# Optimization experiments

Measured on AMD Instinct MI355X. Metric: run time of the kernel, lower is better.

## Reference

```python
import jax, jax.numpy as jnp
import numpy as np

P = 2; NH = 16; HS = 1024; NL = 12; NC = 1000
B, D, H, W = 32, 64, 32, 32
LFEAT = P * P * D  # 256 per-patch feature dim


def _sincos_1d(dim, pos):
    omega = np.arange(dim // 2, dtype=np.float64) / (dim / 2.0)
    omega = 1.0 / 10000 ** omega
    out = np.einsum('m,d->md', pos.reshape(-1), omega)
    return np.concatenate([np.sin(out), np.cos(out)], axis=1)


def _pos_embed(dim, grid_size):
    g = np.arange(grid_size, dtype=np.float32)
    grid = np.stack(np.meshgrid(g, g), axis=0).reshape(2, 1, grid_size, grid_size)
    emb = np.concatenate([_sincos_1d(dim // 2, grid[0]), _sincos_1d(dim // 2, grid[1])], axis=1)
    return jnp.asarray(emb, dtype=jnp.float32)


def setup_inputs() -> dict:
    key = jax.random.key(0)
    ks = iter(jax.random.split(key, 40))
    def w(shape, s=0.02):
        return jax.random.normal(next(ks), shape, jnp.float32) * s
    return {
        'x': jax.random.normal(next(ks), (B, D, H, W), jnp.float32),
        'y': jax.random.randint(next(ks), (B,), 0, NC),
        't': jax.random.randint(next(ks), (B,), 0, 1000),
        'proj_w': w((LFEAT, HS)), 'proj_b': jnp.zeros((HS,), jnp.float32),
        'pos_embed': _pos_embed(HS, H // P),
        'emb_table': w((NC + 1, HS)),
        'blk_mod_w': w((NL, HS, 6 * HS)), 'blk_mod_b': jnp.zeros((NL, 6 * HS), jnp.float32),
        'blk_wq': w((NL, HS, HS)), 'blk_bq': jnp.zeros((NL, HS), jnp.float32),
        'blk_wk': w((NL, HS, HS)), 'blk_bk': jnp.zeros((NL, HS), jnp.float32),
        'blk_wv': w((NL, HS, HS)), 'blk_bv': jnp.zeros((NL, HS), jnp.float32),
        'blk_wo': w((NL, HS, HS)), 'blk_bo': jnp.zeros((NL, HS), jnp.float32),
        'blk_fc1_w': w((NL, HS, 4 * HS)), 'blk_fc1_b': jnp.zeros((NL, 4 * HS), jnp.float32),
        'blk_fc2_w': w((NL, 4 * HS, HS)), 'blk_fc2_b': jnp.zeros((NL, HS), jnp.float32),
        'fin_mod_w': w((HS, 2 * HS)), 'fin_mod_b': jnp.zeros((2 * HS,), jnp.float32),
        'fin_out_w': w((HS, LFEAT)), 'fin_out_b': jnp.zeros((LFEAT,), jnp.float32),
    }


def _ln(z):
    mu = jnp.mean(z, -1, keepdims=True)
    var = jnp.mean((z - mu) ** 2, -1, keepdims=True)
    return (z - mu) * jax.lax.rsqrt(var + 1e-5)


def _forward(x, y, t, proj_w, proj_b, pos_embed, emb_table,
             blk_mod_w, blk_mod_b, blk_wq, blk_bq, blk_wk, blk_bk, blk_wv, blk_bv,
             blk_wo, blk_bo, blk_fc1_w, blk_fc1_b, blk_fc2_w, blk_fc2_b,
             fin_mod_w, fin_mod_b, fin_out_w, fin_out_b):
    Bc, Dc, Hc, Wc = x.shape
    Hp, Wp = Hc // P, Wc // P
    dh = HS // NH
    # patchify_flatten: (B, L, P*P*D)
    tok = x.reshape(Bc, Dc, Hp, P, Wp, P).transpose(0, 2, 4, 3, 5, 1).reshape(Bc, Hp * Wp, P * P * Dc)
    tok = tok @ proj_w + proj_b + pos_embed[None]
    # timestep_embedding: [cos, sin] order per source
    half = HS // 2
    freqs = jnp.exp(-jnp.log(jnp.float32(10000.0)) * jnp.arange(half, dtype=jnp.float32) / half)
    ang = t.astype(jnp.float32)[:, None] * freqs[None]
    c = jnp.concatenate([jnp.cos(ang), jnp.sin(ang)], axis=-1) + emb_table[y]
    c_act = jax.nn.silu(c)  # each block applies silu to c (c is not mutated across blocks)

    def block(xc, p):
        mw, mb, wq, bq, wk, bk, wv, bv, wo, bo, f1w, f1b, f2w, f2b = p
        mod = c_act @ mw + mb
        sh_a, sc_a, g_a, sh_m, sc_m, g_m = jnp.split(mod, 6, axis=1)
        hx = _ln(xc) * (1 + sc_a[:, None]) + sh_a[:, None]
        def heads(z, wz, bz):
            return (z @ wz + bz).reshape(Bc, -1, NH, dh).transpose(0, 2, 1, 3)
        q, k, v = heads(hx, wq, bq), heads(hx, wk, bk), heads(hx, wv, bv)
        logits = jnp.einsum('bhqd,bhkd->bhqk', q, k) / jnp.sqrt(jnp.float32(dh))
        # non-AR mask buffer is all zeros -> no-op
        attn = jax.nn.softmax(logits, axis=-1)
        o = jnp.einsum('bhqk,bhkd->bhqd', attn, v).transpose(0, 2, 1, 3).reshape(Bc, -1, HS)
        xc = xc + g_a[:, None] * (o @ wo + bo)
        hx = _ln(xc) * (1 + sc_m[:, None]) + sh_m[:, None]
        mlp = jax.nn.gelu(hx @ f1w + f1b, approximate=False) @ f2w + f2b
        return xc + g_m[:, None] * mlp, None

    tok, _ = jax.lax.scan(block, tok, (blk_mod_w, blk_mod_b, blk_wq, blk_bq, blk_wk, blk_bk,
                                       blk_wv, blk_bv, blk_wo, blk_bo,
                                       blk_fc1_w, blk_fc1_b, blk_fc2_w, blk_fc2_b))
    fmod = c_act @ fin_mod_w + fin_mod_b
    sh, sc = jnp.split(fmod, 2, axis=1)
    out = (_ln(tok) * (1 + sc[:, None]) + sh[:, None]) @ fin_out_w + fin_out_b
    # unpatchify -> (B, D, H, W)
    return out.reshape(Bc, Hp, Wp, P, P, Dc).transpose(0, 5, 1, 3, 2, 4).reshape(Bc, Dc, Hc, Wc)


def reference(x, y, t, proj_w, proj_b, pos_embed, emb_table,
              blk_mod_w, blk_mod_b, blk_wq, blk_bq, blk_wk, blk_bk, blk_wv, blk_bv,
              blk_wo, blk_bo, blk_fc1_w, blk_fc1_b, blk_fc2_w, blk_fc2_b,
              fin_mod_w, fin_mod_b, fin_out_w, fin_out_b):
    return _forward(x, y, t, proj_w, proj_b, pos_embed, emb_table,
                    blk_mod_w, blk_mod_b, blk_wq, blk_bq, blk_wk, blk_bk, blk_wv, blk_bv,
                    blk_wo, blk_bo, blk_fc1_w, blk_fc1_b, blk_fc2_w, blk_fc2_b,
                    fin_mod_w, fin_mod_b, fin_out_w, fin_out_b)
```

## Files before the change

kernel.cpp:

```cpp
#include <hip/hip_runtime.h>
#include <hip/hip_bf16.h>
#include <math.h>

typedef short s16x8 __attribute__((ext_vector_type(8)));
typedef float f32x4 __attribute__((ext_vector_type(4)));
typedef unsigned short u16;

__device__ __forceinline__ u16 f2b(float f) {
    unsigned u = __builtin_bit_cast(unsigned, f);
    u += 0x7fffu + ((u >> 16) & 1u);
    return (u16)(u >> 16);
}
__device__ __forceinline__ float b2f(u16 h) {
    unsigned u = ((unsigned)h) << 16;
    return __builtin_bit_cast(float, u);
}
__device__ __forceinline__ f32x4 mfma16(s16x8 a, s16x8 b, f32x4 c) {
    return __builtin_amdgcn_mfma_f32_16x16x32_bf16(a, b, c, 0, 0, 0);
}
__device__ __forceinline__ void gload16(const void* g, void* l) {
    __builtin_amdgcn_global_load_lds((const __attribute__((address_space(1))) unsigned*)g,
                                     (__attribute__((address_space(3))) unsigned*)l, 16, 0, 0);
}

__global__ __launch_bounds__(256) void patchify_kernel(const float* __restrict__ x, u16* __restrict__ out) {
    int idx = blockIdx.x * 256 + threadIdx.x;
    int row = idx >> 8, col = idx & 255;
    int b = row >> 8, ll = row & 255, hp = ll >> 4, wp = ll & 15;
    int pp = col >> 6, d = col & 63;
    out[idx] = f2b(x[(size_t)((b * 64 + d) * 32 + hp * 2 + (pp >> 1)) * 32 + wp * 2 + (pp & 1)]);
}

__global__ __launch_bounds__(256) void cact_kernel(const int* __restrict__ t, const int* __restrict__ y,
                                                   const float* __restrict__ emb, u16* __restrict__ cact) {
    int b = blockIdx.x, tid = threadIdx.x;
    float tv = (float)t[b];
    int yb = y[b];
#pragma unroll
    for (int j = 0; j < 4; ++j) {
        int c = tid * 4 + j;
        int f = (c < 512) ? c : c - 512;
        float freq = __expf(-9.210340371976184f * (float)f * (1.f / 512.f));
        float ang = tv * freq;
        float v = (c < 512) ? cosf(ang) : sinf(ang);
        v += emb[(size_t)yb * 1024 + c];
        v = v / (1.f + __expf(-v));
        cact[b * 1024 + c] = f2b(v);
    }
}

__global__ __launch_bounds__(256) void bcat_kernel(const float* __restrict__ bq, const float* __restrict__ bk,
                                                   const float* __restrict__ bv, float* __restrict__ out) {
    int lyr = blockIdx.x, j = blockIdx.y, tid = threadIdx.x;
    const float* src = (j == 0) ? bq : ((j == 1) ? bk : bv);
    float4 v = ((const float4*)(src + (size_t)lyr * 1024))[tid];
    ((float4*)(out + (size_t)lyr * 3072 + j * 1024))[tid] = v;
}

__global__ __launch_bounds__(256) void transpose_cvt(const float* __restrict__ in, u16* __restrict__ out,
                                                     int R, int C) {
    __shared__ float tile[32][33];
    int c0 = blockIdx.x * 32, r0 = blockIdx.y * 32;
    int tid = threadIdx.x;
#pragma unroll
    for (int j = 0; j < 4; ++j) {
        int i = tid + j * 256;
        int r = i >> 5, c = i & 31;
        tile[r][c] = in[(size_t)(r0 + r) * C + c0 + c];
    }
    __syncthreads();
#pragma unroll
    for (int j = 0; j < 4; ++j) {
        int i = tid + j * 256;
        int r = i >> 5, c = i & 31;
        out[(size_t)(c0 + r) * R + r0 + c] = f2b(tile[c][r]);
    }
}

__global__ __launch_bounds__(256) void ln_mod_kernel(const float* __restrict__ x, const float* __restrict__ modv,
                                                     int mod_ld, int sh_off, int sc_off, u16* __restrict__ out) {
    int row = blockIdx.x, tid = threadIdx.x, b = row >> 8;
    float4 xv = ((const float4*)(x + (size_t)row * 1024))[tid];
    float s = xv.x + xv.y + xv.z + xv.w;
    float s2 = xv.x * xv.x + xv.y * xv.y + xv.z * xv.z + xv.w * xv.w;
#pragma unroll
    for (int d = 1; d < 64; d <<= 1) { s += __shfl_xor(s, d); s2 += __shfl_xor(s2, d); }
    __shared__ float red[8];
    int w = tid >> 6;
    if ((tid & 63) == 0) { red[w] = s; red[4 + w] = s2; }
    __syncthreads();
    s = red[0] + red[1] + red[2] + red[3];
    s2 = red[4] + red[5] + red[6] + red[7];
    float mu = s * (1.f / 1024.f);
    float rs = rsqrtf(s2 * (1.f / 1024.f) - mu * mu + 1e-5f);
    const float* shp = modv + (size_t)b * mod_ld + sh_off;
    const float* scp = modv + (size_t)b * mod_ld + sc_off;
    float4 sh4 = ((const float4*)shp)[tid];
    float4 sc4 = ((const float4*)scp)[tid];
    u16 o0 = f2b((xv.x - mu) * rs * (1.f + sc4.x) + sh4.x);
    u16 o1 = f2b((xv.y - mu) * rs * (1.f + sc4.y) + sh4.y);
    u16 o2 = f2b((xv.z - mu) * rs * (1.f + sc4.z) + sh4.z);
    u16 o3 = f2b((xv.w - mu) * rs * (1.f + sc4.w) + sh4.w);
    unsigned long long pk = (unsigned long long)o0 | ((unsigned long long)o1 << 16) |
                            ((unsigned long long)o2 << 32) | ((unsigned long long)o3 << 48);
    *(unsigned long long*)&out[(size_t)row * 1024 + tid * 4] = pk;
}

template <int EPI>
__global__ __launch_bounds__(256, 2) void gemm_k(
    const u16* __restrict__ A, int lda, const u16* __restrict__ Bt, int ldb,
    int M, int N, int K, const float* __restrict__ bias,
    float* outF, u16* __restrict__ outB, int ldc,
    const float* aux1, const float* __restrict__ aux2, int gateOff) {
    __shared__ u16 As[128 * 32];
    __shared__ u16 Bs[128 * 32];
    const int tid = threadIdx.x, w = tid >> 6, l = tid & 63;
    const int row0 = blockIdx.y * 128, col0 = blockIdx.x * 128;
    const int wm = w >> 1, wn = w & 1;

    f32x4 acc[4][4];
#pragma unroll
    for (int m = 0; m < 4; ++m)
#pragma unroll
        for (int n = 0; n < 4; ++n) acc[m][n] = (f32x4){0.f, 0.f, 0.f, 0.f};

    const int rA0 = w * 16 + (l >> 2), rA1 = rA0 + 64;
    const int kc = (l & 3) * 8;
    int gr0 = row0 + rA0; if (gr0 > M - 1) gr0 = M - 1;
    int gr1 = row0 + rA1; if (gr1 > M - 1) gr1 = M - 1;
    const u16* a0 = A + (size_t)gr0 * lda + kc;
    const u16* a1 = A + (size_t)gr1 * lda + kc;
    const u16* b0 = Bt + (size_t)(col0 + rA0) * ldb + kc;
    const u16* b1 = Bt + (size_t)(col0 + rA1) * ldb + kc;
    u16* la0 = &As[rA0 * 32 + kc];
    u16* la1 = &As[rA1 * 32 + kc];
    u16* lb0 = &Bs[rA0 * 32 + kc];
    u16* lb1 = &Bs[rA1 * 32 + kc];

    for (int k0 = 0; k0 < K; k0 += 32) {
        __syncthreads();
        gload16(a0 + k0, la0);
        gload16(a1 + k0, la1);
        gload16(b0 + k0, lb0);
        gload16(b1 + k0, lb1);
        __syncthreads();
        s16x8 af[4], bfr[4];
#pragma unroll
        for (int m = 0; m < 4; ++m)
            af[m] = *(const s16x8*)&As[(wm * 64 + m * 16 + (l & 15)) * 32 + (l >> 4) * 8];
#pragma unroll
        for (int n = 0; n < 4; ++n)
            bfr[n] = *(const s16x8*)&Bs[(wn * 64 + n * 16 + (l & 15)) * 32 + (l >> 4) * 8];
#pragma unroll
        for (int m = 0; m < 4; ++m)
#pragma unroll
            for (int n = 0; n < 4; ++n) acc[m][n] = mfma16(af[m], bfr[n], acc[m][n]);
    }

#pragma unroll
    for (int m = 0; m < 4; ++m) {
#pragma unroll
        for (int n = 0; n < 4; ++n) {
#pragma unroll
            for (int r = 0; r < 4; ++r) {
                int row = row0 + wm * 64 + m * 16 + (l >> 4) * 4 + r;
                if (row >= M) continue;
                int col = col0 + wn * 64 + n * 16 + (l & 15);
                float v = acc[m][n][r];
                if constexpr (EPI == 0) {
                    outF[(size_t)row * ldc + col] = v + bias[col];
                } else if constexpr (EPI == 1) {
                    outB[(size_t)row * ldc + col] = f2b(v + bias[col]);
                } else if constexpr (EPI == 2) {
                    outF[(size_t)row * ldc + col] = v + bias[col] + aux1[(size_t)(row & 255) * 1024 + col];
                } else if constexpr (EPI == 3) {
                    outF[(size_t)row * ldc + col] =
                        aux1[(size_t)row * ldc + col] +
                        aux2[(size_t)(row >> 8) * 6144 + gateOff + col] * (v + bias[col]);
                } else if constexpr (EPI == 4) {
                    float xg = v + bias[col];
                    outB[(size_t)row * ldc + col] = f2b(0.5f * xg * (1.f + erff(xg * 0.70710678118654752f)));
                } else {
                    float xg = v + bias[col];
                    int bb = row >> 8, ll = row & 255, hp = ll >> 4, wp = ll & 15;
                    int pp = col >> 6, d = col & 63;
                    outF[(size_t)((bb * 64 + d) * 32 + hp * 2 + (pp >> 1)) * 32 + wp * 2 + (pp & 1)] = xg;
                }
            }
        }
    }
}

__global__ __launch_bounds__(256, 2) void attn_kernel(const u16* __restrict__ qkv, u16* __restrict__ obuf) {
    __shared__ u16 Qs[64 * 64];
    __shared__ u16 Ks[256 * 64];
    __shared__ u16 VTs[64 * 256];
    int qt = blockIdx.x, h = blockIdx.y, b = blockIdx.z;
    int tid = threadIdx.x, w = tid >> 6, l = tid & 63;
    size_t base = (size_t)b * 256 * 3072;

    {
        int r = tid >> 2;
#pragma unroll
        for (int j = 0; j < 2; ++j) {
            int sg = (tid & 3) + j * 4;
            *(s16x8*)&Qs[r * 64 + sg * 8] =
                *(const s16x8*)&qkv[base + (size_t)(qt * 64 + r) * 3072 + h * 64 + sg * 8];
        }
    }
#pragma unroll
    for (int j = 0; j < 8; ++j) {
        int i = tid + j * 256;
        int r = i >> 3, sg = i & 7;
        *(s16x8*)&Ks[r * 64 + sg * 8] =
            *(const s16x8*)&qkv[base + (size_t)r * 3072 + 1024 + h * 64 + sg * 8];
    }
#pragma unroll
    for (int j = 0; j < 8; ++j) {
        int i = tid + j * 256;
        int r = i >> 3, sg = i & 7;
        s16x8 v = *(const s16x8*)&qkv[base + (size_t)r * 3072 + 2048 + h * 64 + sg * 8];
#pragma unroll
        for (int e = 0; e < 8; ++e) VTs[(sg * 8 + e) * 256 + r] = ((const u16*)&v)[e];
    }
    __syncthreads();

    s16x8 aq0 = *(const s16x8*)&Qs[(w * 16 + (l & 15)) * 64 + (l >> 4) * 8];
    s16x8 aq1 = *(const s16x8*)&Qs[(w * 16 + (l & 15)) * 64 + 32 + (l >> 4) * 8];
    f32x4 sf[16];
#pragma unroll
    for (int cf = 0; cf < 16; ++cf) {
        f32x4 a = (f32x4){0.f, 0.f, 0.f, 0.f};
        s16x8 bk0 = *(const s16x8*)&Ks[(cf * 16 + (l & 15)) * 64 + (l >> 4) * 8];
        s16x8 bk1 = *(const s16x8*)&Ks[(cf * 16 + (l & 15)) * 64 + 32 + (l >> 4) * 8];
        a = mfma16(aq0, bk0, a);
        a = mfma16(aq1, bk1, a);
        sf[cf] = a * 0.125f;
    }
    __syncthreads();

#pragma unroll
    for (int r = 0; r < 4; ++r) {
        float m = -1e30f;
#pragma unroll
        for (int cf = 0; cf < 16; ++cf) m = fmaxf(m, sf[cf][r]);
#pragma unroll
        for (int d = 1; d < 16; d <<= 1) m = fmaxf(m, __shfl_xor(m, d));
        float sm = 0.f;
#pragma unroll
        for (int cf = 0; cf < 16; ++cf) { float e = __expf(sf[cf][r] - m); sf[cf][r] = e; sm += e; }
#pragma unroll
        for (int d = 1; d < 16; d <<= 1) sm += __shfl_xor(sm, d);
        float inv = 1.f / sm;
        int rl = w * 16 + (l >> 4) * 4 + r;
#pragma unroll
        for (int cf = 0; cf < 16; ++cf) Ks[rl * 256 + cf * 16 + (l & 15)] = f2b(sf[cf][r] * inv);
    }
    __syncthreads();

    f32x4 oacc[4];
#pragma unroll
    for (int cf = 0; cf < 4; ++cf) oacc[cf] = (f32x4){0.f, 0.f, 0.f, 0.f};
#pragma unroll
    for (int ks = 0; ks < 8; ++ks) {
        s16x8 ap = *(const s16x8*)&Ks[(w * 16 + (l & 15)) * 256 + ks * 32 + (l >> 4) * 8];
#pragma unroll
        for (int cf = 0; cf < 4; ++cf) {
            s16x8 bv = *(const s16x8*)&VTs[(cf * 16 + (l & 15)) * 256 + ks * 32 + (l >> 4) * 8];
            oacc[cf] = mfma16(ap, bv, oacc[cf]);
        }
    }
    size_t orow0 = (size_t)(b * 256 + qt * 64 + w * 16);
#pragma unroll
    for (int cf = 0; cf < 4; ++cf)
#pragma unroll
        for (int r = 0; r < 4; ++r) {
            int rr = (l >> 4) * 4 + r;
            obuf[(orow0 + rr) * 1024 + h * 64 + cf * 16 + (l & 15)] = f2b(oacc[cf][r]);
        }
}

extern "C" void kernel_launch(void* const* d_in, const int* in_sizes, int n_in,
                              void* d_out, int out_size, void* d_ws, size_t ws_size,
                              hipStream_t stream) {
    (void)in_sizes; (void)n_in; (void)out_size; (void)ws_size;
    const float* x         = (const float*)d_in[0];
    const int*   y         = (const int*)d_in[1];
    const int*   t         = (const int*)d_in[2];
    const float* proj_w    = (const float*)d_in[3];
    const float* proj_b    = (const float*)d_in[4];
    const float* pos_embed = (const float*)d_in[5];
    const float* emb_table = (const float*)d_in[6];
    const float* blk_mod_w = (const float*)d_in[7];
    const float* blk_mod_b = (const float*)d_in[8];
    const float* blk_wq    = (const float*)d_in[9];
    const float* blk_bq    = (const float*)d_in[10];
    const float* blk_wk    = (const float*)d_in[11];
    const float* blk_bk    = (const float*)d_in[12];
    const float* blk_wv    = (const float*)d_in[13];
    const float* blk_bv    = (const float*)d_in[14];
    const float* blk_wo    = (const float*)d_in[15];
    const float* blk_bo    = (const float*)d_in[16];
    const float* blk_f1w   = (const float*)d_in[17];
    const float* blk_f1b   = (const float*)d_in[18];
    const float* blk_f2w   = (const float*)d_in[19];
    const float* blk_f2b   = (const float*)d_in[20];
    const float* fin_mod_w = (const float*)d_in[21];
    const float* fin_mod_b = (const float*)d_in[22];
    const float* fin_out_w = (const float*)d_in[23];
    const float* fin_out_b = (const float*)d_in[24];
    float* out = (float*)d_out;

    char* ws = (char*)d_ws;
    size_t off = 0;
    auto alloc = [&](size_t bytes) -> char* {
        char* p = ws + off;
        off += (bytes + 255) & ~(size_t)255;
        return p;
    };
    float* xc    = (float*)alloc(8192ull * 1024 * 4);
    u16*   hx    = (u16*)alloc(8192ull * 1024 * 2);
    u16*   qkvb  = (u16*)alloc(8192ull * 3072 * 2);
    u16*   obufp = (u16*)alloc(8192ull * 1024 * 2);
    u16*   h1    = (u16*)alloc(8192ull * 4096 * 2);
    u16*   patchA= (u16*)alloc(8192ull * 256 * 2);
    u16*   cact  = (u16*)alloc(32ull * 1024 * 2);
    float* modb  = (float*)alloc(32ull * 6144 * 4);
    float* fmod  = (float*)alloc(32ull * 2048 * 4);
    float* bqkv  = (float*)alloc(12ull * 3072 * 4);
    u16*   projT = (u16*)alloc(1024ull * 256 * 2);
    u16*   fmT   = (u16*)alloc(2048ull * 1024 * 2);
    u16*   foT   = (u16*)alloc(256ull * 1024 * 2);
    u16*   modT  = (u16*)alloc(6144ull * 1024 * 2);
    u16*   qkvT  = (u16*)alloc(3072ull * 1024 * 2);
    u16*   woT   = (u16*)alloc(1024ull * 1024 * 2);
    u16*   f1T   = (u16*)alloc(4096ull * 1024 * 2);
    u16*   f2T   = (u16*)alloc(1024ull * 4096 * 2);

    patchify_kernel<<<8192, 256, 0, stream>>>(x, patchA);
    cact_kernel<<<32, 256, 0, stream>>>(t, y, emb_table, cact);
    bcat_kernel<<<dim3(12, 3), 256, 0, stream>>>(blk_bq, blk_bk, blk_bv, bqkv);
    transpose_cvt<<<dim3(32, 8), 256, 0, stream>>>(proj_w, projT, 256, 1024);
    transpose_cvt<<<dim3(64, 32), 256, 0, stream>>>(fin_mod_w, fmT, 1024, 2048);
    transpose_cvt<<<dim3(8, 32), 256, 0, stream>>>(fin_out_w, foT, 1024, 256);

    gemm_k<2><<<dim3(8, 64), 256, 0, stream>>>(patchA, 256, projT, 256, 8192, 1024, 256,
                                               proj_b, xc, nullptr, 1024, pos_embed, nullptr, 0);
    gemm_k<0><<<dim3(16, 1), 256, 0, stream>>>(cact, 1024, fmT, 1024, 32, 2048, 1024,
                                               fin_mod_b, fmod, nullptr, 2048, nullptr, nullptr, 0);

    for (int i = 0; i < 12; ++i) {
        transpose_cvt<<<dim3(192, 32), 256, 0, stream>>>(blk_mod_w + (size_t)i * 1024 * 6144, modT, 1024, 6144);
        transpose_cvt<<<dim3(32, 32), 256, 0, stream>>>(blk_wq + (size_t)i * 1024 * 1024, qkvT, 1024, 1024);
        transpose_cvt<<<dim3(32, 32), 256, 0, stream>>>(blk_wk + (size_t)i * 1024 * 1024, qkvT + 1024 * 1024, 1024, 1024);
        transpose_cvt<<<dim3(32, 32), 256, 0, stream>>>(blk_wv + (size_t)i * 1024 * 1024, qkvT + 2048 * 1024, 1024, 1024);
        transpose_cvt<<<dim3(32, 32), 256, 0, stream>>>(blk_wo + (size_t)i * 1024 * 1024, woT, 1024, 1024);
        transpose_cvt<<<dim3(128, 32), 256, 0, stream>>>(blk_f1w + (size_t)i * 1024 * 4096, f1T, 1024, 4096);
        transpose_cvt<<<dim3(32, 128), 256, 0, stream>>>(blk_f2w + (size_t)i * 4096 * 1024, f2T, 4096, 1024);

        gemm_k<0><<<dim3(48, 1), 256, 0, stream>>>(cact, 1024, modT, 1024, 32, 6144, 1024,
                                                   blk_mod_b + (size_t)i * 6144, modb, nullptr, 6144,
                                                   nullptr, nullptr, 0);
        ln_mod_kernel<<<8192, 256, 0, stream>>>(xc, modb, 6144, 0, 1024, hx);
        gemm_k<1><<<dim3(24, 64), 256, 0, stream>>>(hx, 1024, qkvT, 1024, 8192, 3072, 1024,
                                                    bqkv + (size_t)i * 3072, nullptr, qkvb, 3072,
                                                    nullptr, nullptr, 0);
        attn_kernel<<<dim3(4, 16, 32), 256, 0, stream>>>(qkvb, obufp);
        gemm_k<3><<<dim3(8, 64), 256, 0, stream>>>(obufp, 1024, woT, 1024, 8192, 1024, 1024,
                                                   blk_bo + (size_t)i * 1024, xc, nullptr, 1024,
                                                   xc, modb, 2048);
        ln_mod_kernel<<<8192, 256, 0, stream>>>(xc, modb, 6144, 3072, 4096, hx);
        gemm_k<4><<<dim3(32, 64), 256, 0, stream>>>(hx, 1024, f1T, 1024, 8192, 4096, 1024,
                                                    blk_f1b + (size_t)i * 4096, nullptr, h1, 4096,
                                                    nullptr, nullptr, 0);
        gemm_k<3><<<dim3(8, 64), 256, 0, stream>>>(h1, 4096, f2T, 4096, 8192, 1024, 4096,
                                                   blk_f2b + (size_t)i * 1024, xc, nullptr, 1024,
                                                   xc, modb, 5120);
    }
    ln_mod_kernel<<<8192, 256, 0, stream>>>(xc, fmod, 2048, 0, 1024, hx);
    gemm_k<5><<<dim3(2, 64), 256, 0, stream>>>(hx, 1024, foT, 1024, 8192, 256, 1024,
                                               fin_out_b, out, nullptr, 256, nullptr, nullptr, 0);
}
```

Baseline: 5.871 ms.

## Add pipelined 256x128 GEMM kernel and fuse per-layer weight transposes

Adds a new 512-thread GEMM with 256x128 tiles, BK=64, triple-buffered LDS, swizzled LDS layout, XCD-aware workgroup remapping, and interleaved async global->LDS loads with MFMA phases. It is used for the large patch-embed, QKV, output-projection and MLP GEMMs. The seven per-layer weight transpose launches become one launch with vectorized 64x64 tiles. The aim is less LDS round-tripping, more load/compute overlap, and fewer launches, at the cost of one block per CU occupancy and hand-tuned waitcnt logic that assumes M, N and K divide the tile sizes.

```diff
diff --git a/kernel.cpp b/kernel.cpp
--- a/kernel.cpp
+++ b/kernel.cpp
@@ -10,10 +10,6 @@
     unsigned u = __builtin_bit_cast(unsigned, f);
     u += 0x7fffu + ((u >> 16) & 1u);
     return (u16)(u >> 16);
-}
-__device__ __forceinline__ float b2f(u16 h) {
-    unsigned u = ((unsigned)h) << 16;
-    return __builtin_bit_cast(float, u);
 }
 __device__ __forceinline__ f32x4 mfma16(s16x8 a, s16x8 b, f32x4 c) {
     return __builtin_amdgcn_mfma_f32_16x16x32_bf16(a, b, c, 0, 0, 0);
@@ -57,24 +53,54 @@
     ((float4*)(out + (size_t)lyr * 3072 + j * 1024))[tid] = v;
 }
 
-__global__ __launch_bounds__(256) void transpose_cvt(const float* __restrict__ in, u16* __restrict__ out,
-                                                     int R, int C) {
-    __shared__ float tile[32][33];
-    int c0 = blockIdx.x * 32, r0 = blockIdx.y * 32;
-    int tid = threadIdx.x;
+__device__ __forceinline__ void tpose_body(float (*tile)[65], const float* __restrict__ in,
+                                           u16* __restrict__ out, int R, int C, int r0, int c0, int tid) {
+    int rr = tid >> 4, cc = (tid & 15) * 4;
 #pragma unroll
     for (int j = 0; j < 4; ++j) {
-        int i = tid + j * 256;
-        int r = i >> 5, c = i & 31;
-        tile[r][c] = in[(size_t)(r0 + r) * C + c0 + c];
+        float4 v = *(const float4*)&in[(size_t)(r0 + j * 16 + rr) * C + c0 + cc];
+        tile[j * 16 + rr][cc]     = v.x;
+        tile[j * 16 + rr][cc + 1] = v.y;
+        tile[j * 16 + rr][cc + 2] = v.z;
+        tile[j * 16 + rr][cc + 3] = v.w;
     }
     __syncthreads();
-#pragma unroll
-    for (int j = 0; j < 4; ++j) {
-        int i = tid + j * 256;
-        int r = i >> 5, c = i & 31;
-        out[(size_t)(c0 + r) * R + r0 + c] = f2b(tile[c][r]);
-    }
+    int oc = tid >> 3, r8 = (tid & 7) * 8;
+#pragma unroll
+    for (int j = 0; j < 2; ++j) {
+        int ocl = j * 32 + oc;
+        s16x8 vv;
+#pragma unroll
+        for (int e = 0; e < 8; ++e) vv[e] = (short)f2b(tile[r8 + e][ocl]);
+        *(s16x8*)&out[(size_t)(c0 + ocl) * R + r0 + r8] = vv;
+    }
+}
+
+__global__ __launch_bounds__(256) void transpose_cvt64k(const float* __restrict__ in, u16* __restrict__ out,
+                                                        int R, int C) {
+    __shared__ float tile[64][65];
+    tpose_body(tile, in, out, R, C, blockIdx.y * 64, blockIdx.x * 64, threadIdx.x);
+}
+
+__global__ __launch_bounds__(256) void transpose_layer(
+    const float* __restrict__ mw, const float* __restrict__ wq, const float* __restrict__ wk,
+    const float* __restrict__ wv, const float* __restrict__ wo, const float* __restrict__ f1,
+    const float* __restrict__ f2,
+    u16* __restrict__ modT, u16* __restrict__ qkvT, u16* __restrict__ woT,
+    u16* __restrict__ f1T, u16* __restrict__ f2T) {
+    __shared__ float tile[64][65];
+    int bid = blockIdx.x, tid = threadIdx.x;
+    const float* src; u16* dst; int R, C, tloc;
+    if (bid < 1536)      { src = mw; dst = modT;               R = 1024; C = 6144; tloc = bid; }
+    else if (bid < 1792) { src = wq; dst = qkvT;               R = 1024; C = 1024; tloc = bid - 1536; }
+    else if (bid < 2048) { src = wk; dst = qkvT + 1024 * 1024; R = 1024; C = 1024; tloc = bid - 1792; }
+    else if (bid < 2304) { src = wv; dst = qkvT + 2048 * 1024; R = 1024; C = 1024; tloc = bid - 2048; }
+    else if (bid < 2560) { src = wo; dst = woT;                R = 1024; C = 1024; tloc = bid - 2304; }
+    else if (bid < 3584) { src = f1; dst = f1T;                R = 1024; C = 4096; tloc = bid - 2560; }
+    else                 { src = f2; dst = f2T;                R = 4096; C = 1024; tloc = bid - 3584; }
+    int tx = C >> 6;
+    int ty = tloc / tx, txi = tloc - ty * tx;
+    tpose_body(tile, src, dst, R, C, ty * 64, txi * 64, tid);
 }
 
 __global__ __launch_bounds__(256) void ln_mod_kernel(const float* __restrict__ x, const float* __restrict__ modv,
@@ -107,13 +133,165 @@
 }
 
 template <int EPI>
+__global__ __launch_bounds__(512, 1) void gemm8(
+    const u16* __restrict__ A, int lda, const u16* __restrict__ Bt, int ldb,
+    int M, int N, int K, const float* __restrict__ bias,
+    float* __restrict__ outF, u16* __restrict__ outB, int ldc,
+    const float* __restrict__ aux1, const float* __restrict__ aux2, int gateOff) {
+    __shared__ u16 As[3][256 * 64];
+    __shared__ u16 Bs[3][128 * 64];
+
+    const int tid = threadIdx.x, w = tid >> 6, l = tid & 63;
+    const int wm = w >> 1, wn = w & 1;
+
+    const int nbn = N >> 7;
+    const int nwg = gridDim.x;
+    const int orig = blockIdx.x;
+    const int cpx = nwg >> 3;
+    const int wg = (orig & 7) * cpx + (orig >> 3);
+    const int bm = wg / nbn, bn = wg - bm * nbn;
+    const int row0 = bm << 8, col0 = bn << 7;
+
+    const int NT = K >> 6;
+
+    const int srow = tid >> 3, sslot = tid & 7;
+    const int ksl = sslot ^ (((srow >> 2) & 1) << 1);
+    const u16* gA = A + (size_t)(row0 + srow) * lda + ksl * 8;
+    const u16* gB = Bt + (size_t)(col0 + srow) * ldb + ksl * 8;
+    const int lOff = srow * 64 + sslot * 8;
+
+    const int fr = l & 15, fg = l >> 4;
+    const int arow = wm * 64 + fr;
+    const int brow = wn * 64 + fr;
+
+    f32x4 acc[4][4];
+#pragma unroll
+    for (int m = 0; m < 4; ++m)
+#pragma unroll
+        for (int n = 0; n < 4; ++n) acc[m][n] = (f32x4){0.f, 0.f, 0.f, 0.f};
+
+    {
+        u16* a0 = &As[0][lOff];
+        u16* b0 = &Bs[0][lOff];
+#pragma unroll
+        for (int a = 0; a < 4; ++a) gload16(gA + (size_t)a * 64 * lda, a0 + a * 4096);
+#pragma unroll
+        for (int b = 0; b < 2; ++b) gload16(gB + (size_t)b * 64 * ldb, b0 + b * 4096);
+        if (NT > 1) {
+            u16* a1 = &As[1][lOff];
+#pragma unroll
+            for (int a = 0; a < 3; ++a) gload16(gA + (size_t)a * 64 * lda + 64, a1 + a * 4096);
+        }
+    }
+    if (NT > 1) { asm volatile("s_waitcnt vmcnt(3)" ::: "memory"); }
+    else        { asm volatile("s_waitcnt vmcnt(0)" ::: "memory"); }
+    __builtin_amdgcn_s_barrier();
+    __builtin_amdgcn_sched_barrier(0);
+
+    int q = 0;
+    for (int t = 0; t < NT; ++t) {
+        const u16* ca = As[q];
+        const u16* cb = Bs[q];
+        const int q1 = (q == 2) ? 0 : q + 1;
+        const int q2 = (q1 == 2) ? 0 : q1 + 1;
+
+        s16x8 af[4][2], bf[4][2];
+#pragma unroll
+        for (int m = 0; m < 4; ++m) {
+            int r = arow + m * 16;
+            int psb = fg ^ (((r >> 2) & 1) << 1);
+            af[m][0] = *(const s16x8*)(ca + r * 64 + psb * 8);
+            af[m][1] = *(const s16x8*)(ca + r * 64 + psb * 8 + 32);
+        }
+#pragma unroll
+        for (int n = 0; n < 2; ++n) {
+            int r = brow + n * 16;
+            int psb = fg ^ (((r >> 2) & 1) << 1);
+            bf[n][0] = *(const s16x8*)(cb + r * 64 + psb * 8);
+            bf[n][1] = *(const s16x8*)(cb + r * 64 + psb * 8 + 32);
+        }
+        if (t + 1 < NT) {
+            gload16(gA + (size_t)(3 * 64) * lda + (size_t)(t + 1) * 64, &As[q1][lOff] + 3 * 4096);
+            gload16(gB + (size_t)(t + 1) * 64, &Bs[q1][lOff]);
+            gload16(gB + (size_t)(1 * 64) * ldb + (size_t)(t + 1) * 64, &Bs[q1][lOff] + 4096);
+        }
+        __builtin_amdgcn_s_barrier();
+        __builtin_amdgcn_s_setprio(1);
+#pragma unroll
+        for (int m = 0; m < 4; ++m)
+#pragma unroll
+            for (int n = 0; n < 2; ++n) {
+                acc[m][n] = mfma16(af[m][0], bf[n][0], acc[m][n]);
+                acc[m][n] = mfma16(af[m][1], bf[n][1], acc[m][n]);
+            }
+        __builtin_amdgcn_s_setprio(0);
+        __builtin_amdgcn_s_barrier();
+#pragma unroll
+        for (int n = 0; n < 2; ++n) {
+            int r = brow + (n + 2) * 16;
+            int psb = fg ^ (((r >> 2) & 1) << 1);
+            bf[n + 2][0] = *(const s16x8*)(cb + r * 64 + psb * 8);
+            bf[n + 2][1] = *(const s16x8*)(cb + r * 64 + psb * 8 + 32);
+        }
+        if (t + 2 < NT) {
+#pragma unroll
+            for (int a = 0; a < 3; ++a)
+                gload16(gA + (size_t)a * 64 * lda + (size_t)(t + 2) * 64, &As[q2][lOff] + a * 4096);
+        }
+        __builtin_amdgcn_s_barrier();
+        __builtin_amdgcn_s_setprio(1);
+#pragma unroll
+        for (int m = 0; m < 4; ++m)
+#pragma unroll
+            for (int n = 2; n < 4; ++n) {
+                acc[m][n] = mfma16(af[m][0], bf[n][0], acc[m][n]);
+                acc[m][n] = mfma16(af[m][1], bf[n][1], acc[m][n]);
+            }
+        __builtin_amdgcn_s_setprio(0);
+        if (t < NT - 2)       { asm volatile("s_waitcnt vmcnt(3)" ::: "memory"); }
+        else if (t == NT - 2) { asm volatile("s_waitcnt vmcnt(0)" ::: "memory"); }
+        if (t < NT - 1) {
+            __builtin_amdgcn_s_barrier();
+            __builtin_amdgcn_sched_barrier(0);
+        }
+        q = q1;
+    }
+
+    const int erow = row0 + wm * 64 + fg * 4;
+    const int ecol = col0 + wn * 64 + fr;
+#pragma unroll
+    for (int m = 0; m < 4; ++m) {
+#pragma unroll
+        for (int n = 0; n < 4; ++n) {
+#pragma unroll
+            for (int r = 0; r < 4; ++r) {
+                int row = erow + m * 16 + r;
+                int col = ecol + n * 16;
+                float v = acc[m][n][r];
+                if constexpr (EPI == 1) {
+                    outB[(size_t)row * ldc + col] = f2b(v + bias[col]);
+                } else if constexpr (EPI == 2) {
+                    outF[(size_t)row * ldc + col] = v + bias[col] + aux1[(size_t)(row & 255) * 1024 + col];
+                } else if constexpr (EPI == 3) {
+                    outF[(size_t)row * ldc + col] =
+                        aux1[(size_t)row * ldc + col] +
+                        aux2[(size_t)(row >> 8) * 6144 + gateOff + col] * (v + bias[col]);
+                } else {
+                    float xg = v + bias[col];
+                    outB[(size_t)row * ldc + col] = f2b(0.5f * xg * (1.f + erff(xg * 0.70710678118654752f)));
+                }
+            }
+        }
+    }
+}
+
+template <int EPI>
 __global__ __launch_bounds__(256, 2) void gemm_k(
     const u16* __restrict__ A, int lda, const u16* __restrict__ Bt, int ldb,
     int M, int N, int K, const float* __restrict__ bias,
-    float* outF, u16* __restrict__ outB, int ldc,
-    const float* aux1, const float* __restrict__ aux2, int gateOff) {
-    __shared__ u16 As[128 * 32];
-    __shared__ u16 Bs[128 * 32];
+    float* outF, u16* __restrict__ outB, int ldc) {
+    __shared__ u16 Asl[128 * 32];
+    __shared__ u16 Bsl[128 * 32];
     const int tid = threadIdx.x, w = tid >> 6, l = tid & 63;
     const int row0 = blockIdx.y * 128, col0 = blockIdx.x * 128;
     const int wm = w >> 1, wn = w & 1;
@@ -132,10 +310,10 @@
     const u16* a1 = A + (size_t)gr1 * lda + kc;
     const u16* b0 = Bt + (size_t)(col0 + rA0) * ldb + kc;
     const u16* b1 = Bt + (size_t)(col0 + rA1) * ldb + kc;
-    u16* la0 = &As[rA0 * 32 + kc];
-    u16* la1 = &As[rA1 * 32 + kc];
-    u16* lb0 = &Bs[rA0 * 32 + kc];
-    u16* lb1 = &Bs[rA1 * 32 + kc];
+    u16* la0 = &Asl[rA0 * 32 + kc];
+    u16* la1 = &Asl[rA1 * 32 + kc];
+    u16* lb0 = &Bsl[rA0 * 32 + kc];
+    u16* lb1 = &Bsl[rA1 * 32 + kc];
 
     for (int k0 = 0; k0 < K; k0 += 32) {
         __syncthreads();
@@ -147,10 +325,10 @@
         s16x8 af[4], bfr[4];
 #pragma unroll
         for (int m = 0; m < 4; ++m)
-            af[m] = *(const s16x8*)&As[(wm * 64 + m * 16 + (l & 15)) * 32 + (l >> 4) * 8];
+            af[m] = *(const s16x8*)&Asl[(wm * 64 + m * 16 + (l & 15)) * 32 + (l >> 4) * 8];
 #pragma unroll
         for (int n = 0; n < 4; ++n)
-            bfr[n] = *(const s16x8*)&Bs[(wn * 64 + n * 16 + (l & 15)) * 32 + (l >> 4) * 8];
+            bfr[n] = *(const s16x8*)&Bsl[(wn * 64 + n * 16 + (l & 15)) * 32 + (l >> 4) * 8];
 #pragma unroll
         for (int m = 0; m < 4; ++m)
 #pragma unroll
@@ -169,17 +347,6 @@
                 float v = acc[m][n][r];
                 if constexpr (EPI == 0) {
                     outF[(size_t)row * ldc + col] = v + bias[col];
-                } else if constexpr (EPI == 1) {
-                    outB[(size_t)row * ldc + col] = f2b(v + bias[col]);
-                } else if constexpr (EPI == 2) {
-                    outF[(size_t)row * ldc + col] = v + bias[col] + aux1[(size_t)(row & 255) * 1024 + col];
-                } else if constexpr (EPI == 3) {
-                    outF[(size_t)row * ldc + col] =
-                        aux1[(size_t)row * ldc + col] +
-                        aux2[(size_t)(row >> 8) * 6144 + gateOff + col] * (v + bias[col]);
-                } else if constexpr (EPI == 4) {
-                    float xg = v + bias[col];
-                    outB[(size_t)row * ldc + col] = f2b(0.5f * xg * (1.f + erff(xg * 0.70710678118654752f)));
                 } else {
                     float xg = v + bias[col];
                     int bb = row >> 8, ll = row & 255, hp = ll >> 4, wp = ll & 15;
@@ -340,44 +507,42 @@
     patchify_kernel<<<8192, 256, 0, stream>>>(x, patchA);
     cact_kernel<<<32, 256, 0, stream>>>(t, y, emb_table, cact);
     bcat_kernel<<<dim3(12, 3), 256, 0, stream>>>(blk_bq, blk_bk, blk_bv, bqkv);
-    transpose_cvt<<<dim3(32, 8), 256, 0, stream>>>(proj_w, projT, 256, 1024);
-    transpose_cvt<<<dim3(64, 32), 256, 0, stream>>>(fin_mod_w, fmT, 1024, 2048);
-    transpose_cvt<<<dim3(8, 32), 256, 0, stream>>>(fin_out_w, foT, 1024, 256);
-
-    gemm_k<2><<<dim3(8, 64), 256, 0, stream>>>(patchA, 256, projT, 256, 8192, 1024, 256,
-                                               proj_b, xc, nullptr, 1024, pos_embed, nullptr, 0);
+    transpose_cvt64k<<<dim3(16, 4), 256, 0, stream>>>(proj_w, projT, 256, 1024);
+    transpose_cvt64k<<<dim3(32, 16), 256, 0, stream>>>(fin_mod_w, fmT, 1024, 2048);
+    transpose_cvt64k<<<dim3(4, 16), 256, 0, stream>>>(fin_out_w, foT, 1024, 256);
+
+    gemm8<2><<<256, 512, 0, stream>>>(patchA, 256, projT, 256, 8192, 1024, 256,
+                                      proj_b, xc, nullptr, 1024, pos_embed, nullptr, 0);
     gemm_k<0><<<dim3(16, 1), 256, 0, stream>>>(cact, 1024, fmT, 1024, 32, 2048, 1024,
-                                               fin_mod_b, fmod, nullptr, 2048, nullptr, nullptr, 0);
+                                               fin_mod_b, fmod, nullptr, 2048);
 
     for (int i = 0; i < 12; ++i) {
-        transpose_cvt<<<dim3(192, 32), 256, 0, stream>>>(blk_mod_w + (size_t)i * 1024 * 6144, modT, 1024, 6144);
-        transpose_cvt<<<dim3(32, 32), 256, 0, stream>>>(blk_wq + (size_t)i * 1024 * 1024, qkvT, 1024, 1024);
-        transpose_cvt<<<dim3(32, 32), 256, 0, stream>>>(blk_wk + (size_t)i * 1024 * 1024, qkvT + 1024 * 1024, 1024, 1024);
-        transpose_cvt<<<dim3(32, 32), 256, 0, stream>>>(blk_wv + (size_t)i * 1024 * 1024, qkvT + 2048 * 1024, 1024, 1024);
-        transpose_cvt<<<dim3(32, 32), 256, 0, stream>>>(blk_wo + (size_t)i * 1024 * 1024, woT, 1024, 1024);
-        transpose_cvt<<<dim3(128, 32), 256, 0, stream>>>(blk_f1w + (size_t)i * 1024 * 4096, f1T, 1024, 4096);
-        transpose_cvt<<<dim3(32, 128), 256, 0, stream>>>(blk_f2w + (size_t)i * 4096 * 1024, f2T, 4096, 1024);
+        transpose_layer<<<4608, 256, 0, stream>>>(
+            blk_mod_w + (size_t)i * 1024 * 6144,
+            blk_wq + (size_t)i * 1024 * 1024, blk_wk + (size_t)i * 1024 * 1024,
+            blk_wv + (size_t)i * 1024 * 1024, blk_wo + (size_t)i * 1024 * 1024,
+            blk_f1w + (size_t)i * 1024 * 4096, blk_f2w + (size_t)i * 4096 * 1024,
+            modT, qkvT, woT, f1T, f2T);
 
         gemm_k<0><<<dim3(48, 1), 256, 0, stream>>>(cact, 1024, modT, 1024, 32, 6144, 1024,
-                                                   blk_mod_b + (size_t)i * 6144, modb, nullptr, 6144,
-                                                   nullptr, nullptr, 0);
+                                                   blk_mod_b + (size_t)i * 6144, modb, nullptr, 6144);
         ln_mod_kernel<<<8192, 256, 0, stream>>>(xc, modb, 6144, 0, 1024, hx);
-        gemm_k<1><<<dim3(24, 64), 256, 0, stream>>>(hx, 1024, qkvT, 1024, 8192, 3072, 1024,
-                                                    bqkv + (size_t)i * 3072, nullptr, qkvb, 3072,
-                                                    nullptr, nullptr, 0);
+        gemm8<1><<<768, 512, 0, stream>>>(hx, 1024, qkvT, 1024, 8192, 3072, 1024,
+                                          bqkv + (size_t)i * 3072, nullptr, qkvb, 3072,
+                                          nullptr, nullptr, 0);
         attn_kernel<<<dim3(4, 16, 32), 256, 0, stream>>>(qkvb, obufp);
-        gemm_k<3><<<dim3(8, 64), 256, 0, stream>>>(obufp, 1024, woT, 1024, 8192, 1024, 1024,
-                                                   blk_bo + (size_t)i * 1024, xc, nullptr, 1024,
-                                                   xc, modb, 2048);
+        gemm8<3><<<256, 512, 0, stream>>>(obufp, 1024, woT, 1024, 8192, 1024, 1024,
+                                          blk_bo + (size_t)i * 1024, xc, nullptr, 1024,
+                                          xc, modb, 2048);
         ln_mod_kernel<<<8192, 256, 0, stream>>>(xc, modb, 6144, 3072, 4096, hx);
-        gemm_k<4><<<dim3(32, 64), 256, 0, stream>>>(hx, 1024, f1T, 1024, 8192, 4096, 1024,
-                                                    blk_f1b + (size_t)i * 4096, nullptr, h1, 4096,
-                                                    nullptr, nullptr, 0);
-        gemm_k<3><<<dim3(8, 64), 256, 0, stream>>>(h1, 4096, f2T, 4096, 8192, 1024, 4096,
-                                                   blk_f2b + (size_t)i * 1024, xc, nullptr, 1024,
-                                                   xc, modb, 5120);
+        gemm8<4><<<1024, 512, 0, stream>>>(hx, 1024, f1T, 1024, 8192, 4096, 1024,
+                                           blk_f1b + (size_t)i * 4096, nullptr, h1, 4096,
+                                           nullptr, nullptr, 0);
+        gemm8<3><<<256, 512, 0, stream>>>(h1, 4096, f2T, 4096, 8192, 1024, 4096,
+                                          blk_f2b + (size_t)i * 1024, xc, nullptr, 1024,
+                                          xc, modb, 5120);
     }
     ln_mod_kernel<<<8192, 256, 0, stream>>>(xc, fmod, 2048, 0, 1024, hx);
     gemm_k<5><<<dim3(2, 64), 256, 0, stream>>>(hx, 1024, foT, 1024, 8192, 256, 1024,
-                                               fin_out_b, out, nullptr, 256, nullptr, nullptr, 0);
-}
+                                               fin_out_b, out, nullptr, 256);
+}
```

After: 5.103 ms. 1.15x faster.
